# Optimization experiments

Measured on AMD Instinct MI355X. Metric: run time of the kernel, lower is better.

Reference implementation:

```python
import jax, jax.numpy as jnp
import numpy as np

EMB = 1024

def setup_inputs() -> dict:
    key = jax.random.key(0)
    ks = jax.random.split(key, 6)
    B, S, E = 4, 2048, EMB
    x = jax.random.normal(ks[0], (B, S, E), dtype=jnp.float32)
    attention_mask = jax.random.randint(ks[1], (B, S, S), 0, 2, dtype=jnp.int32)
    proj_w = jax.random.normal(ks[2], (E, 3 * E), dtype=jnp.float32) * (1.0 / np.sqrt(E))
    proj_b = jax.random.normal(ks[3], (3 * E,), dtype=jnp.float32) * 0.02
    out_w = jax.random.normal(ks[4], (E, E), dtype=jnp.float32) * (1.0 / np.sqrt(E))
    out_b = jax.random.normal(ks[5], (E,), dtype=jnp.float32) * 0.02
    return {"x": x, "attention_mask": attention_mask, "proj_w": proj_w,
            "proj_b": proj_b, "out_w": out_w, "out_b": out_b}

def reference(x, attention_mask, proj_w, proj_b, out_w, out_b):
    E = x.shape[-1]
    scale = 1.0 / jnp.sqrt(jnp.asarray(E, x.dtype))
    qkv = x @ proj_w + proj_b                      # [B,S,3E]
    q, k, v = jnp.split(qkv, 3, axis=-1)           # each [B,S,E]
    scores = jnp.einsum('bqe,bke->bqk', q, k) * scale  # [B,S,S]
    scores = jnp.where(attention_mask == 0, jnp.asarray(-1e20, scores.dtype), scores)
    attn = jax.nn.softmax(scores, axis=-1)
    ctx = jnp.einsum('bqk,bke->bqe', attn, v)      # [B,S,E]
    return ctx @ out_w + out_b
```

## Files before the change

kernel.cpp:

```cpp
#include <hip/hip_runtime.h>
#include <cstdint>

typedef unsigned short u16;
typedef uint32_t u32;
typedef __bf16 bf16x8 __attribute__((ext_vector_type(8)));
typedef float f32x4 __attribute__((ext_vector_type(4)));

__device__ __forceinline__ u16 f2bf(float f) {
  unsigned u = __float_as_uint(f);
  u += 0x7fffu + ((u >> 16) & 1u);
  return (u16)(u >> 16);
}

__device__ __forceinline__ void async16(const void* g, void* l) {
  __builtin_amdgcn_global_load_lds(
      (const __attribute__((address_space(1))) uint32_t*)g,
      (__attribute__((address_space(3))) uint32_t*)l, 16, 0, 0);
}

__global__ __launch_bounds__(256) void k_prep(const float* __restrict__ x, u16* __restrict__ xb,
                                              const float* __restrict__ pw, u16* __restrict__ wt,
                                              const float* __restrict__ ow, u16* __restrict__ owt,
                                              const int* __restrict__ mask, u32* __restrict__ mbits) {
  const int bid = blockIdx.x;
  if (bid < 8192) {
    const int i = bid * 256 + threadIdx.x;
    const float4 v = ((const float4*)x)[i];
    ushort4 o;
    o.x = f2bf(v.x); o.y = f2bf(v.y); o.z = f2bf(v.z); o.w = f2bf(v.w);
    ((ushort4*)xb)[i] = o;
    return;
  }
  if (bid >= 12288) {
    const size_t w = (size_t)(bid - 12288) * 256 + threadIdx.x;
    const int* p = mask + w * 32;
    u32 bits = 0;
#pragma unroll
    for (int j = 0; j < 8; ++j) {
      const int4 v = ((const int4*)p)[j];
      bits |= (u32)(v.x & 1) << (j * 4 + 0);
      bits |= (u32)(v.y & 1) << (j * 4 + 1);
      bits |= (u32)(v.z & 1) << (j * 4 + 2);
      bits |= (u32)(v.w & 1) << (j * 4 + 3);
    }
    mbits[w] = bits;
    return;
  }
  __shared__ u16 tile[32][33];
  const int tx = threadIdx.x & 31, ty = threadIdx.x >> 5;
  const float* in;
  u16* outp;
  int lda, ldo, c0, r0;
  if (bid < 11264) {
    const int id = bid - 8192;
    c0 = (id % 96) * 32; r0 = (id / 96) * 32;
    in = pw; outp = wt; lda = 3072; ldo = 1024;
  } else {
    const int id = bid - 11264;
    c0 = (id % 32) * 32; r0 = (id / 32) * 32;
    in = ow; outp = owt; lda = 1024; ldo = 1024;
  }
#pragma unroll
  for (int i = 0; i < 4; ++i)
    tile[ty + i * 8][tx] = f2bf(in[(size_t)(r0 + ty + i * 8) * lda + c0 + tx]);
  __syncthreads();
#pragma unroll
  for (int i = 0; i < 4; ++i)
    outp[(size_t)(c0 + ty + i * 8) * ldo + r0 + tx] = tile[tx][ty + i * 8];
}

template <int MODE, int TM, int BN>
__device__ __forceinline__ void gemm_core(
    u16* As, u16* Bs,
    const u16* __restrict__ A, long lda, long bsA,
    const u16* __restrict__ Bt, long ldb, long bsB,
    void* __restrict__ C, long ldc, long bsC,
    int M, int N, int K,
    const float* __restrict__ bias, const u32* __restrict__ mbits,
    int b, int bx, int by) {
  constexpr int MT = TM / 32, NT = BN / 32;
  constexpr int ACALLS = TM / 8, TOT = (TM + BN) / 8, NC = TOT / 4;
  const int m0 = by * TM, n0 = bx * BN;
  const int lane = threadIdx.x & 63;
  const int w = threadIdx.x >> 6;
  const int wr = w >> 1, wc = w & 1;

  const int srow = lane >> 3;
  const int scol = ((lane & 7) ^ ((lane >> 3) & 7)) * 8;
  const u16* pa = A + (size_t)b * bsA + (size_t)(m0 + srow) * lda + scol;
  const u16* pb = Bt + (size_t)b * bsB + (size_t)(n0 + srow) * ldb + scol;

  const int m_l = lane & 15, q = lane >> 4, m7 = m_l & 7;
  const int offs[2] = {(q ^ m7) * 8, ((4 + q) ^ m7) * 8};

  f32x4 acc[MT][NT] = {};
  f32x4 accs[MT] = {};
  bf16x8 ones;
#pragma unroll
  for (int e = 0; e < 8; ++e) ones[e] = (__bf16)1.0f;

  for (int kt = 0; kt < K; kt += 64) {
    __syncthreads();
#pragma unroll
    for (int g = 0; g < NC; ++g) {
      const int idx = w * NC + g;
      if (idx < ACALLS)
        async16(pa + (size_t)(idx * 8) * lda, As + idx * 512);
      else
        async16(pb + (size_t)((idx - ACALLS) * 8) * ldb, Bs + (idx - ACALLS) * 512);
    }
    __syncthreads();
#pragma unroll
    for (int s = 0; s < 2; ++s) {
      bf16x8 af[MT], bfr[NT];
#pragma unroll
      for (int t = 0; t < MT; ++t)
        af[t] = *(const bf16x8*)(As + (wr * (TM / 2) + t * 16 + m_l) * 64 + offs[s]);
#pragma unroll
      for (int t = 0; t < NT; ++t)
        bfr[t] = *(const bf16x8*)(Bs + (wc * (BN / 2) + t * 16 + m_l) * 64 + offs[s]);
#pragma unroll
      for (int mt = 0; mt < MT; ++mt)
#pragma unroll
        for (int nt = 0; nt < NT; ++nt)
          acc[mt][nt] = __builtin_amdgcn_mfma_f32_16x16x32_bf16(af[mt], bfr[nt], acc[mt][nt], 0, 0, 0);
      if constexpr (MODE == 2) {
#pragma unroll
        for (int mt = 0; mt < MT; ++mt)
          accs[mt] = __builtin_amdgcn_mfma_f32_16x16x32_bf16(af[mt], ones, accs[mt], 0, 0, 0);
      }
    }
    pa += 64;
    pb += 64;
  }

  if constexpr (MODE == 1) {
    __syncthreads();
    const int rl = threadIdx.x >> 1, pr = threadIdx.x & 1;
    const uint2 v = *(const uint2*)(mbits + ((size_t)(b * M + m0 + rl)) * (N >> 5) + (n0 >> 5) + pr * 2);
    ((u32*)As)[rl * 4 + pr * 2] = v.x;
    ((u32*)As)[rl * 4 + pr * 2 + 1] = v.y;
    __syncthreads();
  }

  float rinv[MT][4];
  if constexpr (MODE == 2) {
#pragma unroll
    for (int mt = 0; mt < MT; ++mt)
#pragma unroll
      for (int r = 0; r < 4; ++r) rinv[mt][r] = 1.0f / accs[mt][r];
  }

#pragma unroll
  for (int mt = 0; mt < MT; ++mt) {
#pragma unroll
    for (int nt = 0; nt < NT; ++nt) {
      const int col = n0 + wc * (BN / 2) + nt * 16 + m_l;
      const int row0 = m0 + wr * (TM / 2) + mt * 16 + q * 4;
      if constexpr (MODE == 3) {
        ushort4 o;
        o.x = f2bf(acc[mt][nt][0]); o.y = f2bf(acc[mt][nt][1]);
        o.z = f2bf(acc[mt][nt][2]); o.w = f2bf(acc[mt][nt][3]);
        *(ushort4*)((u16*)C + (size_t)b * bsC + (size_t)col * ldc + row0) = o;
      } else {
#pragma unroll
        for (int r = 0; r < 4; ++r) {
          const int row = row0 + r;
          float v = acc[mt][nt][r];
          if constexpr (MODE == 0) {
            v += bias[col];
            if (col < 1024) v *= 0.03125f;
            ((u16*)C)[(size_t)b * bsC + (size_t)row * ldc + col] = f2bf(v);
          } else if constexpr (MODE == 1) {
            const int cl = wc * 64 + nt * 16 + m_l;
            const int rl = wr * 64 + mt * 16 + q * 4 + r;
            const u32 wb = ((const u32*)As)[rl * 4 + (cl >> 5)];
            v = ((wb >> (cl & 31)) & 1u) ? __expf(fminf(v, 30.f)) : 0.f;
            ((u16*)C)[(size_t)b * bsC + (size_t)row * ldc + col] = f2bf(v);
          } else if constexpr (MODE == 2) {
            v = v * rinv[mt][r] + bias[col];
            ((float*)C)[(size_t)b * bsC + (size_t)row * ldc + col] = v;
          }
        }
      }
    }
  }
}

template <int MODE, int TM, int BN>
__global__ __launch_bounds__(256) void gemm_bt(
    const u16* __restrict__ A, long lda, long bsA,
    const u16* __restrict__ Bt, long ldb, long bsB,
    void* __restrict__ C, long ldc, long bsC,
    int M, int N, int K,
    const float* __restrict__ bias, const u32* __restrict__ mbits) {
  __shared__ u16 As[TM * 64];
  __shared__ u16 Bs[BN * 64];
  gemm_core<MODE, TM, BN>(As, Bs, A, lda, bsA, Bt, ldb, bsB, C, ldc, bsC, M, N, K,
                          bias, mbits, blockIdx.z, blockIdx.x, blockIdx.y);
}

__global__ __launch_bounds__(256) void k_mid(
    const u16* __restrict__ qkv, u16* __restrict__ P, u16* __restrict__ Ut,
    const u16* __restrict__ owt, const u32* __restrict__ mbits) {
  __shared__ u16 As[128 * 64];
  __shared__ u16 Bs[128 * 64];
  const int z = blockIdx.z;
  if (z < 4) {
    gemm_core<1, 128, 128>(As, Bs,
        qkv, 3072, (long)2048 * 3072, qkv + 1024, 3072, (long)2048 * 3072,
        P, 2048, (long)2048 * 2048, 2048, 2048, 1024, nullptr, mbits,
        z, blockIdx.x, blockIdx.y);
  } else {
    if (blockIdx.x >= 8) return;
    gemm_core<3, 128, 128>(As, Bs,
        qkv + 2048, 3072, (long)2048 * 3072, owt, 1024, 0,
        Ut, 2048, (long)1024 * 2048, 2048, 1024, 1024, nullptr, nullptr,
        z - 4, blockIdx.x, blockIdx.y);
  }
}

extern "C" void kernel_launch(void* const* d_in, const int* in_sizes, int n_in,
                              void* d_out, int out_size, void* d_ws, size_t ws_size,
                              hipStream_t stream) {
  const float* x = (const float*)d_in[0];
  const int* mask = (const int*)d_in[1];
  const float* proj_w = (const float*)d_in[2];
  const float* proj_b = (const float*)d_in[3];
  const float* out_w = (const float*)d_in[4];
  const float* out_b = (const float*)d_in[5];
  float* out = (float*)d_out;

  char* ws = (char*)d_ws;
  u16* xb = (u16*)(ws);
  u16* wt = (u16*)(ws + 16777216);
  u16* owt = (u16*)(ws + 23068672);
  u16* qkv = (u16*)(ws + 25165824);
  u16* P = (u16*)(ws + 75497472);
  u32* mbits = (u32*)(ws + 109051904);
  u16* Ut = (u16*)xb;

  k_prep<<<14336, 256, 0, stream>>>(x, xb, proj_w, wt, out_w, owt, mask, mbits);
  gemm_bt<0, 128, 128><<<dim3(24, 64, 1), 256, 0, stream>>>(
      xb, 1024, 0, wt, 1024, 0, qkv, 3072, 0, 8192, 3072, 1024, proj_b, nullptr);
  k_mid<<<dim3(16, 16, 8), 256, 0, stream>>>(qkv, P, Ut, owt, mbits);
  gemm_bt<2, 64, 64><<<dim3(16, 32, 4), 256, 0, stream>>>(
      P, 2048, (long)2048 * 2048, Ut, 2048, (long)1024 * 2048,
      out, 1024, (long)2048 * 1024, 2048, 1024, 2048, out_b, nullptr);
}
```

Before: 379.8 us.

## Fuse all stages into a persistent megakernel with grid-wide barriers

Replaces the four separate launches (prep, QKV GEMM, scores/V·Wo GEMM, output GEMM) with a single persistent kernel of 512 blocks. Work units are distributed in grid-stride loops, and the stages are separated by atomic-counter grid barriers. Tile shapes for the V·Wo and final GEMM stages also change to 64x128. The aim is to remove launch gaps and tail idle time between stages. In exchange it relies on all 512 blocks being co-resident and on counter reset and initialisation ordering across repeated calls, since a stale magic value could let blocks pass barriers early.

After: 778.1 us. 2.05x slower.

```diff
diff --git a/kernel.cpp b/kernel.cpp
--- a/kernel.cpp
+++ b/kernel.cpp
@@ -6,6 +6,8 @@
 typedef __bf16 bf16x8 __attribute__((ext_vector_type(8)));
 typedef float f32x4 __attribute__((ext_vector_type(4)));
 
+#define NB 512
+
 __device__ __forceinline__ u16 f2bf(float f) {
   unsigned u = __float_as_uint(f);
   u += 0x7fffu + ((u >> 16) & 1u);
@@ -18,55 +20,16 @@
       (__attribute__((address_space(3))) uint32_t*)l, 16, 0, 0);
 }
 
-__global__ __launch_bounds__(256) void k_prep(const float* __restrict__ x, u16* __restrict__ xb,
-                                              const float* __restrict__ pw, u16* __restrict__ wt,
-                                              const float* __restrict__ ow, u16* __restrict__ owt,
-                                              const int* __restrict__ mask, u32* __restrict__ mbits) {
-  const int bid = blockIdx.x;
-  if (bid < 8192) {
-    const int i = bid * 256 + threadIdx.x;
-    const float4 v = ((const float4*)x)[i];
-    ushort4 o;
-    o.x = f2bf(v.x); o.y = f2bf(v.y); o.z = f2bf(v.z); o.w = f2bf(v.w);
-    ((ushort4*)xb)[i] = o;
-    return;
-  }
-  if (bid >= 12288) {
-    const size_t w = (size_t)(bid - 12288) * 256 + threadIdx.x;
-    const int* p = mask + w * 32;
-    u32 bits = 0;
-#pragma unroll
-    for (int j = 0; j < 8; ++j) {
-      const int4 v = ((const int4*)p)[j];
-      bits |= (u32)(v.x & 1) << (j * 4 + 0);
-      bits |= (u32)(v.y & 1) << (j * 4 + 1);
-      bits |= (u32)(v.z & 1) << (j * 4 + 2);
-      bits |= (u32)(v.w & 1) << (j * 4 + 3);
-    }
-    mbits[w] = bits;
-    return;
-  }
-  __shared__ u16 tile[32][33];
-  const int tx = threadIdx.x & 31, ty = threadIdx.x >> 5;
-  const float* in;
-  u16* outp;
-  int lda, ldo, c0, r0;
-  if (bid < 11264) {
-    const int id = bid - 8192;
-    c0 = (id % 96) * 32; r0 = (id / 96) * 32;
-    in = pw; outp = wt; lda = 3072; ldo = 1024;
-  } else {
-    const int id = bid - 11264;
-    c0 = (id % 32) * 32; r0 = (id / 32) * 32;
-    in = ow; outp = owt; lda = 1024; ldo = 1024;
-  }
-#pragma unroll
-  for (int i = 0; i < 4; ++i)
-    tile[ty + i * 8][tx] = f2bf(in[(size_t)(r0 + ty + i * 8) * lda + c0 + tx]);
+__device__ __forceinline__ void gbarrier(u32* c) {
   __syncthreads();
-#pragma unroll
-  for (int i = 0; i < 4; ++i)
-    outp[(size_t)(c0 + ty + i * 8) * ldo + r0 + tx] = tile[tx][ty + i * 8];
+  __threadfence();
+  if (threadIdx.x == 0) {
+    __hip_atomic_fetch_add(c, 1u, __ATOMIC_ACQ_REL, __HIP_MEMORY_SCOPE_AGENT);
+    while (__hip_atomic_load(c, __ATOMIC_ACQUIRE, __HIP_MEMORY_SCOPE_AGENT) < NB)
+      __builtin_amdgcn_s_sleep(1);
+  }
+  __syncthreads();
+  __threadfence();
 }
 
 template <int MODE, int TM, int BN>
@@ -187,37 +150,108 @@
   }
 }
 
-template <int MODE, int TM, int BN>
-__global__ __launch_bounds__(256) void gemm_bt(
-    const u16* __restrict__ A, long lda, long bsA,
-    const u16* __restrict__ Bt, long ldb, long bsB,
-    void* __restrict__ C, long ldc, long bsC,
-    int M, int N, int K,
-    const float* __restrict__ bias, const u32* __restrict__ mbits) {
-  __shared__ u16 As[TM * 64];
-  __shared__ u16 Bs[BN * 64];
-  gemm_core<MODE, TM, BN>(As, Bs, A, lda, bsA, Bt, ldb, bsB, C, ldc, bsC, M, N, K,
-                          bias, mbits, blockIdx.z, blockIdx.x, blockIdx.y);
-}
-
-__global__ __launch_bounds__(256) void k_mid(
-    const u16* __restrict__ qkv, u16* __restrict__ P, u16* __restrict__ Ut,
-    const u16* __restrict__ owt, const u32* __restrict__ mbits) {
+__global__ __launch_bounds__(256, 2) void k_mega(
+    const float* __restrict__ x, const int* __restrict__ mask,
+    const float* __restrict__ pw, const float* __restrict__ pb,
+    const float* __restrict__ ow, const float* __restrict__ ob,
+    float* __restrict__ out, char* __restrict__ ws) {
   __shared__ u16 As[128 * 64];
   __shared__ u16 Bs[128 * 64];
-  const int z = blockIdx.z;
-  if (z < 4) {
-    gemm_core<1, 128, 128>(As, Bs,
-        qkv, 3072, (long)2048 * 3072, qkv + 1024, 3072, (long)2048 * 3072,
-        P, 2048, (long)2048 * 2048, 2048, 2048, 1024, nullptr, mbits,
-        z, blockIdx.x, blockIdx.y);
-  } else {
-    if (blockIdx.x >= 8) return;
-    gemm_core<3, 128, 128>(As, Bs,
-        qkv + 2048, 3072, (long)2048 * 3072, owt, 1024, 0,
-        Ut, 2048, (long)1024 * 2048, 2048, 1024, 1024, nullptr, nullptr,
-        z - 4, blockIdx.x, blockIdx.y);
-  }
+  u16* xb = (u16*)(ws);
+  u16* wt = (u16*)(ws + 16777216);
+  u16* owt = (u16*)(ws + 23068672);
+  u16* qkv = (u16*)(ws + 25165824);
+  u16* P = (u16*)(ws + 75497472);
+  u32* mbits = (u32*)(ws + 109051904);
+  u32* cnt = (u32*)(ws + 111149056);
+  u16* Ut = xb;
+  const int bid = blockIdx.x;
+
+  if (bid == 0 && threadIdx.x == 0) {
+    __hip_atomic_store(&cnt[1], 0u, __ATOMIC_RELAXED, __HIP_MEMORY_SCOPE_AGENT);
+    __hip_atomic_store(&cnt[2], 0u, __ATOMIC_RELAXED, __HIP_MEMORY_SCOPE_AGENT);
+    __hip_atomic_store(&cnt[3], 0u, __ATOMIC_RELAXED, __HIP_MEMORY_SCOPE_AGENT);
+    __hip_atomic_store(&cnt[0], 0xC0FFEEu, __ATOMIC_RELEASE, __HIP_MEMORY_SCOPE_AGENT);
+  }
+  if (threadIdx.x == 0) {
+    while (__hip_atomic_load(&cnt[0], __ATOMIC_ACQUIRE, __HIP_MEMORY_SCOPE_AGENT) != 0xC0FFEEu)
+      __builtin_amdgcn_s_sleep(1);
+  }
+  __syncthreads();
+
+  for (int u = bid; u < 14336; u += NB) {
+    if (u < 8192) {
+      const int i = u * 256 + threadIdx.x;
+      const float4 v = ((const float4*)x)[i];
+      ushort4 o;
+      o.x = f2bf(v.x); o.y = f2bf(v.y); o.z = f2bf(v.z); o.w = f2bf(v.w);
+      ((ushort4*)xb)[i] = o;
+    } else if (u >= 12288) {
+      const size_t wd = (size_t)(u - 12288) * 256 + threadIdx.x;
+      const int* p = mask + wd * 32;
+      u32 bits = 0;
+#pragma unroll
+      for (int j = 0; j < 8; ++j) {
+        const int4 v = ((const int4*)p)[j];
+        bits |= (u32)(v.x & 1) << (j * 4 + 0);
+        bits |= (u32)(v.y & 1) << (j * 4 + 1);
+        bits |= (u32)(v.z & 1) << (j * 4 + 2);
+        bits |= (u32)(v.w & 1) << (j * 4 + 3);
+      }
+      mbits[wd] = bits;
+    } else {
+      u16(*tile)[33] = (u16(*)[33])As;
+      const int tx = threadIdx.x & 31, ty = threadIdx.x >> 5;
+      const float* in;
+      u16* outp;
+      int lda, ldo, c0, r0;
+      if (u < 11264) {
+        const int id = u - 8192;
+        c0 = (id % 96) * 32; r0 = (id / 96) * 32;
+        in = pw; outp = wt; lda = 3072; ldo = 1024;
+      } else {
+        const int id = u - 11264;
+        c0 = (id % 32) * 32; r0 = (id / 32) * 32;
+        in = ow; outp = owt; lda = 1024; ldo = 1024;
+      }
+#pragma unroll
+      for (int i = 0; i < 4; ++i)
+        tile[ty + i * 8][tx] = f2bf(in[(size_t)(r0 + ty + i * 8) * lda + c0 + tx]);
+      __syncthreads();
+#pragma unroll
+      for (int i = 0; i < 4; ++i)
+        outp[(size_t)(c0 + ty + i * 8) * ldo + r0 + tx] = tile[tx][ty + i * 8];
+      __syncthreads();
+    }
+  }
+  gbarrier(&cnt[1]);
+
+  for (int t = bid; t < 1536; t += NB)
+    gemm_core<0, 128, 128>(As, Bs, xb, 1024, 0, wt, 1024, 0, qkv, 3072, 0,
+                           8192, 3072, 1024, pb, nullptr, 0, t % 24, t / 24);
+  gbarrier(&cnt[2]);
+
+  for (int t = bid; t < 2048; t += NB) {
+    if (t < 1024) {
+      gemm_core<1, 128, 128>(As, Bs,
+          qkv, 3072, (long)2048 * 3072, qkv + 1024, 3072, (long)2048 * 3072,
+          P, 2048, (long)2048 * 2048, 2048, 2048, 1024, nullptr, mbits,
+          t >> 8, t & 15, (t >> 4) & 15);
+    } else {
+      const int t2 = t - 1024;
+      gemm_core<3, 64, 128>(As, Bs,
+          qkv + 2048, 3072, (long)2048 * 3072, owt, 1024, 0,
+          Ut, 2048, (long)1024 * 2048, 2048, 1024, 1024, nullptr, nullptr,
+          t2 >> 8, t2 & 7, (t2 >> 3) & 31);
+    }
+  }
+  gbarrier(&cnt[3]);
+
+  for (int t = bid; t < 1024; t += NB)
+    gemm_core<2, 64, 128>(As, Bs,
+        P, 2048, (long)2048 * 2048, Ut, 2048, (long)1024 * 2048,
+        out, 1024, (long)2048 * 1024, 2048, 1024, 2048, ob, nullptr,
+        t >> 8, t & 7, (t >> 3) & 31);
 }
 
 extern "C" void kernel_launch(void* const* d_in, const int* in_sizes, int n_in,
@@ -231,20 +265,5 @@
   const float* out_b = (const float*)d_in[5];
   float* out = (float*)d_out;
 
-  char* ws = (char*)d_ws;
-  u16* xb = (u16*)(ws);
-  u16* wt = (u16*)(ws + 16777216);
-  u16* owt = (u16*)(ws + 23068672);
-  u16* qkv = (u16*)(ws + 25165824);
-  u16* P = (u16*)(ws + 75497472);
-  u32* mbits = (u32*)(ws + 109051904);
-  u16* Ut = (u16*)xb;
-
-  k_prep<<<14336, 256, 0, stream>>>(x, xb, proj_w, wt, out_w, owt, mask, mbits);
-  gemm_bt<0, 128, 128><<<dim3(24, 64, 1), 256, 0, stream>>>(
-      xb, 1024, 0, wt, 1024, 0, qkv, 3072, 0, 8192, 3072, 1024, proj_b, nullptr);
-  k_mid<<<dim3(16, 16, 8), 256, 0, stream>>>(qkv, P, Ut, owt, mbits);
-  gemm_bt<2, 64, 64><<<dim3(16, 32, 4), 256, 0, stream>>>(
-      P, 2048, (long)2048 * 2048, Ut, 2048, (long)1024 * 2048,
-      out, 1024, (long)2048 * 1024, 2048, 1024, 2048, out_b, nullptr);
-}
+  k_mega<<<NB, 256, 0, stream>>>(x, mask, proj_w, proj_b, out_w, out_b, out, (char*)d_ws);
+}
```
